# Kernel optimization log

Hardware: AMD Instinct MI355X
Metric: run time of the kernel (lower is better)

## Reference

```python
import jax, jax.numpy as jnp
import numpy as np
from jax import lax

VOCAB, D, LAYERS, PAD = 10000, 200, 3, 3
B, S = 16, 512
SCALE = 0.05  # ~ torch uniform(-1/sqrt(200), 1/sqrt(200)) scale


def setup_inputs() -> dict:
    key = jax.random.key(0)
    ks = jax.random.split(key, 8)
    x = jax.random.randint(ks[0], (B, S), 0, VOCAB)
    emb = jax.random.normal(ks[1], (VOCAB, D), jnp.float32) * SCALE
    emb = emb.at[PAD].set(0.0)  # padding_idx=3 row is zeros
    w_ih = jax.random.normal(ks[2], (LAYERS, D, D), jnp.float32) * SCALE
    w_hh = jax.random.normal(ks[3], (LAYERS, D, D), jnp.float32) * SCALE
    b_ih = jax.random.normal(ks[4], (LAYERS, D), jnp.float32) * SCALE
    b_hh = jax.random.normal(ks[5], (LAYERS, D), jnp.float32) * SCALE
    fc_w = jax.random.normal(ks[6], (VOCAB, D), jnp.float32) * SCALE
    fc_b = jax.random.normal(ks[7], (VOCAB,), jnp.float32) * SCALE
    return {"x": x, "emb": emb, "w_ih": w_ih, "w_hh": w_hh,
            "b_ih": b_ih, "b_hh": b_hh, "fc_w": fc_w, "fc_b": fc_b}


def _rnn_forward(x, emb, w_ih, w_hh, b_ih, b_hh, fc_w, fc_b):
    h = emb[x]  # (B, S, D) embedding gather
    finals = []
    for l in range(LAYERS):
        # precompute input projection for the whole sequence (efficient GEMM)
        xw = jnp.einsum('bsd,hd->bsh', h, w_ih[l]) + b_ih[l] + b_hh[l]  # (B,S,D)
        w_hh_l_T = w_hh[l].T

        def step(h_prev, x_t):
            h_new = jnp.tanh(x_t + h_prev @ w_hh_l_T)
            return h_new, h_new

        h0 = jnp.zeros((x.shape[0], D), xw.dtype)
        h_last, outs = lax.scan(step, h0, jnp.swapaxes(xw, 0, 1))  # scan over time
        h = jnp.swapaxes(outs, 0, 1)  # (B, S, D)
        finals.append(h_last)
    hidden = jnp.stack(finals)  # (LAYERS, B, D) like torch RNN hidden
    logits = h @ fc_w.T + fc_b  # (B, S, VOCAB)
    return logits, hidden


def reference(x, emb, w_ih, w_hh, b_ih, b_hh, fc_w, fc_b):
    # forward always starts from zero hidden (source ignores the hidden arg)
    return _rnn_forward(x, emb, w_ih, w_hh, b_ih, b_hh, fc_w, fc_b)
```

## Files before the change

kernel.cpp:

```cpp
#include <hip/hip_runtime.h>
#include <hip/hip_bf16.h>

#define VOCAB 10000
#define D 200
#define NLAYERS 3
#define NB 16
#define NS 512
#define M 8192
#define KA 224
#define KB 232
#define NPADA 10120
#define NTILES_N 79

#define OFF_BUF0 0u
#define OFF_BUF1 6553600u
#define OFF_WT   13107200u
#define OFF_HBF  13587200u
#define OFF_FWB  17257216u
#define OFF_STG1 21952896u
#define WS_NEED  28506496u

typedef __bf16 bf16x8 __attribute__((ext_vector_type(8)));
typedef float  f32x4  __attribute__((ext_vector_type(4)));
typedef unsigned int u32x4 __attribute__((ext_vector_type(4)));

__global__ void k_embed(const int* __restrict__ x, const float* __restrict__ emb,
                        float* __restrict__ h0) {
    int i = blockIdx.x * blockDim.x + threadIdx.x;
    if (i < M * D) {
        int bs = i / D;
        int d  = i - bs * D;
        h0[i] = emb[(size_t)x[bs] * D + d];
    }
}

__global__ void k_wtrans(const float* __restrict__ w_ih, float* __restrict__ wt) {
    int i = blockIdx.x * blockDim.x + threadIdx.x;
    if (i < NLAYERS * D * D) {
        int l = i / (D * D);
        int r = i - l * D * D;
        int k = r / D;
        int n = r - k * D;
        wt[i] = w_ih[l * D * D + n * D + k];
    }
}

__global__ void k_fcwbf(const float* __restrict__ fc_w, __bf16* __restrict__ fwb) {
    int i = blockIdx.x * blockDim.x + threadIdx.x;
    if (i < NPADA * KB) {
        int n = i / KB;
        int k = i - n * KB;
        float v = (n < VOCAB && k < D) ? fc_w[(size_t)n * D + k] : 0.f;
        fwb[i] = (__bf16)v;
    }
}

__global__ void k_hbf2(const float* __restrict__ h, __bf16* __restrict__ hbf) {
    int i = blockIdx.x * blockDim.x + threadIdx.x;
    if (i < M * KA) {
        int m = i / KA;
        int k = i - m * KA;
        float v = (k < D) ? h[(size_t)m * D + k] : 0.f;
        hbf[i] = (__bf16)v;
    }
}

__global__ void k_zero(u32x4* __restrict__ p, int n4) {
    int i = blockIdx.x * blockDim.x + threadIdx.x;
    if (i < n4) p[i] = u32x4{0u, 0u, 0u, 0u};
}

__global__ void k_xw(const float* __restrict__ hin, const float* __restrict__ wt,
                     const float* __restrict__ b_ih, const float* __restrict__ b_hh,
                     float* __restrict__ xw) {
    int m0 = blockIdx.x * 32;
    int n  = threadIdx.x;
    if (n >= D) return;
    float bias = b_ih[n] + b_hh[n];
    for (int g = 0; g < 8; ++g) {
        const float* r0 = hin + (size_t)(m0 + g * 4) * D;
        float a0 = bias, a1 = bias, a2 = bias, a3 = bias;
        for (int k = 0; k < D; k += 4) {
            #pragma unroll
            for (int kk = 0; kk < 4; ++kk) {
                float w = wt[(k + kk) * D + n];
                float h0v = r0[k + kk];
                float h1v = r0[D + k + kk];
                float h2v = r0[2 * D + k + kk];
                float h3v = r0[3 * D + k + kk];
                a0 += h0v * w; a1 += h1v * w; a2 += h2v * w; a3 += h3v * w;
            }
        }
        size_t o = (size_t)(m0 + g * 4) * D + n;
        xw[o] = a0; xw[o + D] = a1; xw[o + 2 * D] = a2; xw[o + 3 * D] = a3;
    }
}

__device__ inline float fast_tanh(float x) {
    x = fminf(fmaxf(x, -15.f), 15.f);
    float e = __expf(2.f * x);
    return (e - 1.f) / (e + 1.f);
}

__global__ __attribute__((amdgpu_flat_work_group_size(512, 512),
                          amdgpu_waves_per_eu(2, 2)))
void k_scan_pipe(const float* __restrict__ whh_all,
                 const float* __restrict__ wih_all,
                 const float* __restrict__ b_ih,
                 const float* __restrict__ b_hh,
                 const float* __restrict__ xw0,
                 unsigned* __restrict__ stage0,
                 unsigned* __restrict__ stage1,
                 __bf16* __restrict__ hbf,
                 float* __restrict__ hidden) {
    __shared__ float hp0[208], hp1[208], hin[208];
    const int bid = blockIdx.x;
    const int l   = bid >> 4;
    const int b   = bid & 15;
    const int t   = threadIdx.x;
    const int q   = t >> 2, dg = t & 3;
    const bool act = (q < 100);
    const int  rr  = 2 * q + (dg & 1);
    const int  rrl = act ? rr : 0;
    const bool wlane = act && (dg < 2);
    const int  dstart = dg * 52;

    f32x4 wh[2][13], wi[2][13];
    #pragma unroll
    for (int j = 0; j < 2; ++j)
        #pragma unroll
        for (int i = 0; i < 13; ++i) {
            wh[j][i] = f32x4{0.f, 0.f, 0.f, 0.f};
            wi[j][i] = f32x4{0.f, 0.f, 0.f, 0.f};
        }
    if (act) {
        #pragma unroll
        for (int j = 0; j < 2; ++j) {
            const float* wr = whh_all + (size_t)l * D * D + (size_t)(2 * q + j) * D + dstart;
            #pragma unroll
            for (int i = 0; i < 11; ++i) wh[j][i] = *(const f32x4*)(wr + 4 * i);
            if (dg < 3) {
                wh[j][11] = *(const f32x4*)(wr + 44);
                wh[j][12] = *(const f32x4*)(wr + 48);
            }
        }
        if (l > 0) {
            #pragma unroll
            for (int j = 0; j < 2; ++j) {
                const float* wr = wih_all + (size_t)l * D * D + (size_t)(2 * q + j) * D + dstart;
                #pragma unroll
                for (int i = 0; i < 11; ++i) wi[j][i] = *(const f32x4*)(wr + 4 * i);
                if (dg < 3) {
                    wi[j][11] = *(const f32x4*)(wr + 44);
                    wi[j][12] = *(const f32x4*)(wr + 48);
                }
            }
        }
    }
    float bias = 0.f;
    if (l > 0 && act) bias = b_ih[l * D + rr] + b_hh[l * D + rr];

    if (t < 208) { hp0[t] = 0.f; hp1[t] = 0.f; hin[t] = 0.f; }
    __syncthreads();

    const float* xrow = xw0 + (size_t)b * NS * D;
    const unsigned* sin = (l == 1) ? stage0 + (size_t)b * NS * 200
                        : (l == 2) ? stage1 + (size_t)b * NS * 200 : nullptr;
    unsigned* sout = (l == 0) ? stage0 + (size_t)b * NS * 200
                   : (l == 1) ? stage1 + (size_t)b * NS * 200 : nullptr;

    float xv_next = (l == 0) ? xrow[rrl] : 0.f;
    float hlast = 0.f;
    const float* hi = hin + dstart;

    #pragma unroll 1
    for (int s = 0; s < NS; ++s) {
        float xv;
        if (l == 0) {
            xv = xv_next;
            const int sn = (s + 1 < NS) ? s + 1 : NS - 1;
            xv_next = xrow[(size_t)sn * D + rrl];
        } else {
            if (t < 200) {
                const unsigned* p = sin + (size_t)s * 200 + t;
                unsigned v;
                do {
                    v = __hip_atomic_load(p, __ATOMIC_RELAXED,
                                          __HIP_MEMORY_SCOPE_AGENT);
                } while (v == 0u);
                hin[t] = __builtin_bit_cast(float, ~v);
            }
            asm volatile("s_waitcnt lgkmcnt(0)" ::: "memory");
            __builtin_amdgcn_s_barrier();
            asm volatile("" ::: "memory");
            xv = bias;
        }
        const float* hr = ((s & 1) ? hp1 : hp0) + dstart;
        float* hw = (s & 1) ? hp0 : hp1;
        f32x4 ac0{0.f,0.f,0.f,0.f}, ac1{0.f,0.f,0.f,0.f};
        #pragma unroll
        for (int i = 0; i < 13; ++i) {
            f32x4 h4 = *(const f32x4*)(hr + 4 * i);
            ac0 += h4 * wh[0][i];
            ac1 += h4 * wh[1][i];
        }
        if (l > 0) {
            #pragma unroll
            for (int i = 0; i < 13; ++i) {
                f32x4 g4 = *(const f32x4*)(hi + 4 * i);
                ac0 += g4 * wi[0][i];
                ac1 += g4 * wi[1][i];
            }
        }
        float s0 = (ac0.x + ac0.y) + (ac0.z + ac0.w);
        float s1 = (ac1.x + ac1.y) + (ac1.z + ac1.w);
        s0 += __shfl_xor(s0, 1);  s0 += __shfl_xor(s0, 2);
        s1 += __shfl_xor(s1, 1);  s1 += __shfl_xor(s1, 2);
        float hn = fast_tanh(xv + ((dg & 1) ? s1 : s0));
        hlast = hn;
        if (wlane) {
            hw[rr] = hn;
            if (l < 2) {
                __hip_atomic_store(sout + (size_t)s * 200 + rr,
                                   ~__builtin_bit_cast(unsigned, hn),
                                   __ATOMIC_RELAXED, __HIP_MEMORY_SCOPE_AGENT);
            } else {
                hbf[((size_t)b * NS + s) * KA + rr] = (__bf16)hn;
            }
        }
        asm volatile("s_waitcnt lgkmcnt(0)" ::: "memory");
        __builtin_amdgcn_s_barrier();
        asm volatile("" ::: "memory");
    }
    if (wlane) hidden[(size_t)l * NB * D + b * D + rr] = hlast;
}

#define STEP(HR, HW, SIDX)                                                  \
    {                                                                       \
        float xv = xv_next;                                                 \
        int snext = (SIDX) + 1 < NS ? (SIDX) + 1 : NS - 1;                  \
        xv_next = xrow[(size_t)snext * D + rrl];                            \
        f32x4 ac0{0.f,0.f,0.f,0.f}, ac1{0.f,0.f,0.f,0.f};                   \
        _Pragma("unroll")                                                   \
        for (int i = 0; i < 13; ++i) {                                      \
            f32x4 h4 = *(const f32x4*)((HR) + 4 * i);                       \
            ac0 += h4 * w4[0][i];                                           \
            ac1 += h4 * w4[1][i];                                           \
        }                                                                   \
        float s0 = (ac0.x + ac0.y) + (ac0.z + ac0.w);                       \
        float s1 = (ac1.x + ac1.y) + (ac1.z + ac1.w);                       \
        s0 += __shfl_xor(s0, 1);  s0 += __shfl_xor(s0, 2);                  \
        s1 += __shfl_xor(s1, 1);  s1 += __shfl_xor(s1, 2);                  \
        float hn = fast_tanh(xv + ((dg & 1) ? s1 : s0));                    \
        hlast = hn;                                                         \
        if (wlane) {                                                        \
            (HW)[rr] = hn;                                                  \
            xrow[(size_t)(SIDX) * D + rr] = hn;                             \
        }                                                                   \
        __syncthreads();                                                    \
    }

__global__ __attribute__((amdgpu_flat_work_group_size(512, 512),
                          amdgpu_waves_per_eu(2, 2)))
void k_scan(const float* __restrict__ whh,
            float* __restrict__ io,
            float* __restrict__ hidden) {
    __shared__ float hp0[208], hp1[208];
    int t  = threadIdx.x;
    int b  = blockIdx.x;
    int q  = t >> 2;
    int dg = t & 3;
    const bool act = (q < 100);
    const int  rr  = 2 * q + (dg & 1);
    const int  rrl = act ? rr : 0;
    const bool wlane = act && (dg < 2);
    const int  dstart = dg * 52;

    f32x4 w4[2][13];
    #pragma unroll
    for (int j = 0; j < 2; ++j)
        #pragma unroll
        for (int i = 0; i < 13; ++i) w4[j][i] = f32x4{0.f, 0.f, 0.f, 0.f};
    if (act) {
        #pragma unroll
        for (int j = 0; j < 2; ++j) {
            const float* wr = whh + (size_t)(2 * q + j) * D + dstart;
            #pragma unroll
            for (int i = 0; i < 11; ++i) w4[j][i] = *(const f32x4*)(wr + 4 * i);
            if (dg < 3) {
                w4[j][11] = *(const f32x4*)(wr + 44);
                w4[j][12] = *(const f32x4*)(wr + 48);
            }
        }
    }
    if (t < 208) { hp0[t] = 0.f; hp1[t] = 0.f; }
    __syncthreads();

    float* xrow = io + (size_t)b * NS * D;
    const float* hr0 = hp0 + dstart;
    const float* hr1 = hp1 + dstart;
    float xv_next = xrow[rrl];
    float hlast = 0.f;

    #pragma unroll 1
    for (int s2 = 0; s2 < NS / 2; ++s2) {
        STEP(hr0, hp1, 2 * s2)
        STEP(hr1, hp0, 2 * s2 + 1)
    }
    if (wlane) hidden[b * D + rr] = hlast;
}

__global__ __launch_bounds__(256) void k_fc(const __bf16* __restrict__ A,
                                            const __bf16* __restrict__ Bw,
                                            const float* __restrict__ fc_b,
                                            float* __restrict__ Cout) {
    __shared__ __bf16 Bl[3840 * 8];
    int tid = threadIdx.x;
    int wg  = blockIdx.x;
    int mt  = wg / NTILES_N, nt = wg - mt * NTILES_N;
    int m0  = mt * 128, n0 = nt * 128;

    {
        const u32x4* src = (const u32x4*)(Bw + (size_t)n0 * KB);
        u32x4* dst = (u32x4*)Bl;
        u32x4 stg[15];
        #pragma unroll
        for (int it = 0; it < 15; ++it) stg[it] = src[tid + it * 256];
        #pragma unroll
        for (int it = 0; it < 15; ++it) dst[tid + it * 256] = stg[it];
    }
    __syncthreads();

    int lane = tid & 63, wv = tid >> 6;
    int wr = wv >> 1, wc = wv & 1;
    int lr = lane & 15, lq = lane >> 4;
    f32x4 acc[4][4] = {};
    #pragma unroll
    for (int ks = 0; ks < 7; ++ks) {
        bf16x8 af[4], bfr[4];
        #pragma unroll
        for (int i = 0; i < 4; ++i) {
            int arow = m0 + wr * 64 + i * 16 + lr;
            af[i] = *(const bf16x8*)(A + (size_t)arow * KA + (ks * 4 + lq) * 8);
            int brow = wc * 64 + i * 16 + lr;
            bfr[i] = *(const bf16x8*)(Bl + brow * KB + (ks * 4 + lq) * 8);
        }
        #pragma unroll
        for (int i = 0; i < 4; ++i) {
            #pragma unroll
            for (int j = 0; j < 4; ++j) {
                acc[i][j] = __builtin_amdgcn_mfma_f32_16x16x32_bf16(af[i], bfr[j],
                                                                   acc[i][j], 0, 0, 0);
            }
        }
    }
    #pragma unroll
    for (int j = 0; j < 4; ++j) {
        int col = n0 + wc * 64 + j * 16 + lr;
        if (col < VOCAB) {
            float bias = fc_b[col];
            #pragma unroll
            for (int i = 0; i < 4; ++i) {
                #pragma unroll
                for (int r = 0; r < 4; ++r) {
                    int row = m0 + wr * 64 + i * 16 + lq * 4 + r;
                    Cout[(size_t)row * VOCAB + col] = acc[i][j][r] + bias;
                }
            }
        }
    }
}

extern "C" void kernel_launch(void* const* d_in, const int* in_sizes, int n_in,
                              void* d_out, int out_size, void* d_ws, size_t ws_size,
                              hipStream_t stream) {
    const int*   x    = (const int*)  d_in[0];
    const float* emb  = (const float*)d_in[1];
    const float* w_ih = (const float*)d_in[2];
    const float* w_hh = (const float*)d_in[3];
    const float* b_ih = (const float*)d_in[4];
    const float* b_hh = (const float*)d_in[5];
    const float* fc_w = (const float*)d_in[6];
    const float* fc_b = (const float*)d_in[7];
    float* out    = (float*)d_out;
    float* hidden = out + (size_t)M * VOCAB;

    char* ws = (char*)d_ws;
    float*    buf0 = (float*)(ws + OFF_BUF0);
    float*    buf1 = (float*)(ws + OFF_BUF1);
    float*    wt   = (float*)(ws + OFF_WT);
    __bf16*   hbf  = (__bf16*)(ws + OFF_HBF);
    __bf16*   fwb  = (__bf16*)(ws + OFF_FWB);
    unsigned* stg0 = (unsigned*)(ws + OFF_BUF0);
    unsigned* stg1 = (unsigned*)(ws + OFF_STG1);

    k_embed <<<(M * D + 255) / 256, 256, 0, stream>>>(x, emb, buf0);
    k_wtrans<<<(NLAYERS * D * D + 255) / 256, 256, 0, stream>>>(w_ih, wt);
    k_fcwbf <<<(NPADA * KB + 255) / 256, 256, 0, stream>>>(fc_w, fwb);

    if (ws_size >= WS_NEED) {
        k_xw<<<M / 32, 256, 0, stream>>>(buf0, wt, b_ih, b_hh, buf1);
        const int nst4 = NB * NS * 200 / 4;
        const int nhb4 = M * KA * 2 / 16;
        k_zero<<<(nst4 + 255) / 256, 256, 0, stream>>>((u32x4*)stg0, nst4);
        k_zero<<<(nst4 + 255) / 256, 256, 0, stream>>>((u32x4*)stg1, nst4);
        k_zero<<<(nhb4 + 255) / 256, 256, 0, stream>>>((u32x4*)hbf, nhb4);
        k_scan_pipe<<<NB * NLAYERS, 512, 0, stream>>>(w_hh, w_ih, b_ih, b_hh,
                                                      buf1, stg0, stg1, hbf, hidden);
    } else {
        float* cur = buf0;
        float* nxt = buf1;
        for (int l = 0; l < NLAYERS; ++l) {
            k_xw  <<<M / 32, 256, 0, stream>>>(cur, wt + l * D * D,
                                               b_ih + l * D, b_hh + l * D, nxt);
            k_scan<<<NB, 512, 0, stream>>>(w_hh + (size_t)l * D * D, nxt,
                                           hidden + l * NB * D);
            float* tswap = cur; cur = nxt; nxt = tswap;
        }
        k_hbf2<<<(M * KA + 255) / 256, 256, 0, stream>>>(cur, hbf);
    }
    k_fc<<<64 * NTILES_N, 256, 0, stream>>>(hbf, fwb, fc_b, out);
}
```

Measured before the change: 866.7 us.

## Fuse embedding gather into input projection, add spin sleep, nontemporal logits stores

Removes the separate embedding kernel and gathers embedding rows directly inside the first-layer input-projection kernel, avoiding a full write and re-read of the embedded activations. The inter-layer spin-wait now sleeps briefly between polls, which may reduce memory contention but adds wake-up latency on the critical recurrent path. The final FC output stores become nontemporal to avoid polluting caches with the large logits tensor. Some variables are renamed without any behaviour change.

```diff
diff --git a/kernel.cpp b/kernel.cpp
--- a/kernel.cpp
+++ b/kernel.cpp
@@ -24,16 +24,6 @@
 typedef float  f32x4  __attribute__((ext_vector_type(4)));
 typedef unsigned int u32x4 __attribute__((ext_vector_type(4)));
 
-__global__ void k_embed(const int* __restrict__ x, const float* __restrict__ emb,
-                        float* __restrict__ h0) {
-    int i = blockIdx.x * blockDim.x + threadIdx.x;
-    if (i < M * D) {
-        int bs = i / D;
-        int d  = i - bs * D;
-        h0[i] = emb[(size_t)x[bs] * D + d];
-    }
-}
-
 __global__ void k_wtrans(const float* __restrict__ w_ih, float* __restrict__ wt) {
     int i = blockIdx.x * blockDim.x + threadIdx.x;
     if (i < NLAYERS * D * D) {
@@ -68,6 +58,33 @@
 __global__ void k_zero(u32x4* __restrict__ p, int n4) {
     int i = blockIdx.x * blockDim.x + threadIdx.x;
     if (i < n4) p[i] = u32x4{0u, 0u, 0u, 0u};
+}
+
+__global__ void k_xw_emb(const int* __restrict__ x, const float* __restrict__ emb,
+                         const float* __restrict__ wt,
+                         const float* __restrict__ b_ih, const float* __restrict__ b_hh,
+                         float* __restrict__ xw) {
+    int m0 = blockIdx.x * 32;
+    int n  = threadIdx.x;
+    if (n >= D) return;
+    float bias = b_ih[n] + b_hh[n];
+    for (int g = 0; g < 8; ++g) {
+        const float* r0 = emb + (size_t)x[m0 + g * 4 + 0] * D;
+        const float* r1 = emb + (size_t)x[m0 + g * 4 + 1] * D;
+        const float* r2 = emb + (size_t)x[m0 + g * 4 + 2] * D;
+        const float* r3 = emb + (size_t)x[m0 + g * 4 + 3] * D;
+        float a0 = bias, a1 = bias, a2 = bias, a3 = bias;
+        for (int k = 0; k < D; k += 4) {
+            #pragma unroll
+            for (int kk = 0; kk < 4; ++kk) {
+                float w = wt[(k + kk) * D + n];
+                a0 += r0[k + kk] * w; a1 += r1[k + kk] * w;
+                a2 += r2[k + kk] * w; a3 += r3[k + kk] * w;
+            }
+        }
+        size_t o = (size_t)(m0 + g * 4) * D + n;
+        xw[o] = a0; xw[o + D] = a1; xw[o + 2 * D] = a2; xw[o + 3 * D] = a3;
+    }
 }
 
 __global__ void k_xw(const float* __restrict__ hin, const float* __restrict__ wt,
@@ -109,8 +126,8 @@
                  const float* __restrict__ b_ih,
                  const float* __restrict__ b_hh,
                  const float* __restrict__ xw0,
-                 unsigned* __restrict__ stage0,
-                 unsigned* __restrict__ stage1,
+                 unsigned* __restrict__ cells1,
+                 unsigned* __restrict__ cells2,
                  __bf16* __restrict__ hbf,
                  float* __restrict__ hidden) {
     __shared__ float hp0[208], hp1[208], hin[208];
@@ -164,13 +181,13 @@
     __syncthreads();
 
     const float* xrow = xw0 + (size_t)b * NS * D;
-    const unsigned* sin = (l == 1) ? stage0 + (size_t)b * NS * 200
-                        : (l == 2) ? stage1 + (size_t)b * NS * 200 : nullptr;
-    unsigned* sout = (l == 0) ? stage0 + (size_t)b * NS * 200
-                   : (l == 1) ? stage1 + (size_t)b * NS * 200 : nullptr;
-
+    const unsigned* sin = (l == 1) ? cells1 + (size_t)b * NS * 200
+                        : (l == 2) ? cells2 + (size_t)b * NS * 200 : nullptr;
+    unsigned* sout = (l == 0) ? cells1 + (size_t)b * NS * 200
+                   : (l == 1) ? cells2 + (size_t)b * NS * 200 : nullptr;
+
+    float hn_prev = 0.f;
     float xv_next = (l == 0) ? xrow[rrl] : 0.f;
-    float hlast = 0.f;
     const float* hi = hin + dstart;
 
     #pragma unroll 1
@@ -183,11 +200,13 @@
         } else {
             if (t < 200) {
                 const unsigned* p = sin + (size_t)s * 200 + t;
-                unsigned v;
-                do {
+                unsigned v = __hip_atomic_load(p, __ATOMIC_RELAXED,
+                                               __HIP_MEMORY_SCOPE_AGENT);
+                while (v == 0u) {
+                    __builtin_amdgcn_s_sleep(1);
                     v = __hip_atomic_load(p, __ATOMIC_RELAXED,
                                           __HIP_MEMORY_SCOPE_AGENT);
-                } while (v == 0u);
+                }
                 hin[t] = __builtin_bit_cast(float, ~v);
             }
             asm volatile("s_waitcnt lgkmcnt(0)" ::: "memory");
@@ -217,7 +236,7 @@
         s0 += __shfl_xor(s0, 1);  s0 += __shfl_xor(s0, 2);
         s1 += __shfl_xor(s1, 1);  s1 += __shfl_xor(s1, 2);
         float hn = fast_tanh(xv + ((dg & 1) ? s1 : s0));
-        hlast = hn;
+        hn_prev = hn;
         if (wlane) {
             hw[rr] = hn;
             if (l < 2) {
@@ -232,7 +251,7 @@
         __builtin_amdgcn_s_barrier();
         asm volatile("" ::: "memory");
     }
-    if (wlane) hidden[(size_t)l * NB * D + b * D + rr] = hlast;
+    if (wlane) hidden[(size_t)l * NB * D + b * D + rr] = hn_prev;
 }
 
 #define STEP(HR, HW, SIDX)                                                  \
@@ -364,7 +383,8 @@
                 #pragma unroll
                 for (int r = 0; r < 4; ++r) {
                     int row = m0 + wr * 64 + i * 16 + lq * 4 + r;
-                    Cout[(size_t)row * VOCAB + col] = acc[i][j][r] + bias;
+                    __builtin_nontemporal_store(acc[i][j][r] + bias,
+                                                &Cout[(size_t)row * VOCAB + col]);
                 }
             }
         }
@@ -394,12 +414,11 @@
     unsigned* stg0 = (unsigned*)(ws + OFF_BUF0);
     unsigned* stg1 = (unsigned*)(ws + OFF_STG1);
 
-    k_embed <<<(M * D + 255) / 256, 256, 0, stream>>>(x, emb, buf0);
     k_wtrans<<<(NLAYERS * D * D + 255) / 256, 256, 0, stream>>>(w_ih, wt);
     k_fcwbf <<<(NPADA * KB + 255) / 256, 256, 0, stream>>>(fc_w, fwb);
 
     if (ws_size >= WS_NEED) {
-        k_xw<<<M / 32, 256, 0, stream>>>(buf0, wt, b_ih, b_hh, buf1);
+        k_xw_emb<<<M / 32, 256, 0, stream>>>(x, emb, wt, b_ih, b_hh, buf1);
         const int nst4 = NB * NS * 200 / 4;
         const int nhb4 = M * KA * 2 / 16;
         k_zero<<<(nst4 + 255) / 256, 256, 0, stream>>>((u32x4*)stg0, nst4);
@@ -408,9 +427,11 @@
         k_scan_pipe<<<NB * NLAYERS, 512, 0, stream>>>(w_hh, w_ih, b_ih, b_hh,
                                                       buf1, stg0, stg1, hbf, hidden);
     } else {
-        float* cur = buf0;
-        float* nxt = buf1;
-        for (int l = 0; l < NLAYERS; ++l) {
+        k_xw_emb<<<M / 32, 256, 0, stream>>>(x, emb, wt, b_ih, b_hh, buf1);
+        k_scan<<<NB, 512, 0, stream>>>(w_hh, buf1, hidden);
+        float* cur = buf1;
+        float* nxt = buf0;
+        for (int l = 1; l < NLAYERS; ++l) {
             k_xw  <<<M / 32, 256, 0, stream>>>(cur, wt + l * D * D,
                                                b_ih + l * D, b_hh + l * D, nxt);
             k_scan<<<NB, 512, 0, stream>>>(w_hh + (size_t)l * D * D, nxt,
```

Result: no change. 854.6 us (-1.4%).
